# Optimization experiments

Hardware: AMD Instinct MI355X
Metric: run time of the kernel (lower is better)

Reference implementation:

```python
import jax, jax.numpy as jnp
import numpy as np

TAU_PRE = 2.0   # pre-synaptic trace time constant
SCALE = 1.0     # forward(scale=1.0) default
SPIKE_P = 0.1   # firing probability for realistic binary spike trains


def setup_inputs() -> dict:
    key = jax.random.key(0)
    k1, k2 = jax.random.split(key)
    T, B, NIN, NOUT = 2048, 128, 256, 128
    # binary spike trains, [T, B, N]
    in_spikes = (jax.random.uniform(k1, (T, B, NIN)) < SPIKE_P).astype(jnp.float32)
    out_spikes = (jax.random.uniform(k2, (T, B, NOUT)) < SPIKE_P).astype(jnp.float32)
    return {"in_spikes": in_spikes, "out_spikes": out_spikes}


def reference(in_spikes, out_spikes):
    # STDP.forward: loop over recorded timesteps, per step:
    #   trace_pre = trace_pre - trace_pre/tau_pre + in_spike          (decayed trace)
    #   dw = sum_b trace_pre[b, :] (outer) out_spike[b, :] -> [NOUT, NIN]
    #   delta_w += scale * dw
    # Expressed as a single lax.scan over the time axis.
    B, NIN = in_spikes.shape[1], in_spikes.shape[2]
    NOUT = out_spikes.shape[2]

    def step(carry, xs):
        trace_pre, delta_w = carry
        s_in, s_out = xs                                 # [B, NIN], [B, NOUT]
        trace_pre = trace_pre - trace_pre / TAU_PRE + s_in
        dw = jnp.einsum('bi,bo->oi', trace_pre, s_out)   # [NOUT, NIN]
        return (trace_pre, delta_w + SCALE * dw), None

    init = (jnp.zeros((B, NIN), in_spikes.dtype),
            jnp.zeros((NOUT, NIN), in_spikes.dtype))
    (_, delta_w), _ = jax.lax.scan(step, init, (in_spikes, out_spikes))
    return delta_w
```

## Files before the change

### kernel.cpp

```cpp
#include <hip/hip_runtime.h>
#include <hip/hip_bf16.h>

#define T_TOTAL 2048
#define BATCH   128
#define NIN     256
#define NOUT    128

#define TC      256
#define BC      4
#define WARM    32
#define NTC     (T_TOTAL / TC)
#define NBC     (BATCH / BC)
#define NBLOCKS (NTC * NBC)
#define SUP     16
#define NSUP    (TC / SUP)

#define OUT_ELEMS (NOUT * NIN)

typedef __attribute__((ext_vector_type(8)))  __bf16 bf16x8;
typedef __attribute__((ext_vector_type(2)))  __bf16 bf16x2;
typedef __attribute__((ext_vector_type(16))) float  f32x16;
typedef __attribute__((ext_vector_type(4)))  unsigned uint32x4;

static __device__ __forceinline__ unsigned pack_bf16(float a, float b) {
    bf16x2 v = { (__bf16)a, (__bf16)b };
    union { bf16x2 v; unsigned u; } c; c.v = v; return c.u;
}

__global__ __launch_bounds__(512, 2)
void stdp_main(const float* __restrict__ in, const float* __restrict__ outs,
               float* __restrict__ dst, int nslots, int use_atomic)
{
    __shared__ __align__(16) unsigned tr_lds[2][NIN * 32];
    __shared__ __align__(16) unsigned ot_lds[2][NOUT * 32];

    const int tid = threadIdx.x;
    const int bc  = blockIdx.x % NBC;
    const int tc  = blockIdx.x / NBC;
    const int b0  = bc * BC;
    const int t0  = tc * TC;

    const int i_idx = tid & 255;
    const int bh    = tid >> 8;
    const int o_idx = tid & 127;
    const int bp    = (tid >> 7) & 1;
    const int th    = (tid >> 8) & 1;

    float tr0 = 0.f, tr1 = 0.f;

    if (tc > 0) {
        for (int t = t0 - WARM; t < t0; t += 8) {
            float v0[8], v1[8];
#pragma unroll
            for (int u = 0; u < 8; ++u) {
                const size_t base = ((size_t)(t + u) * BATCH + b0 + 2 * bh) * NIN + i_idx;
                v0[u] = in[base];
                v1[u] = in[base + NIN];
            }
#pragma unroll
            for (int u = 0; u < 8; ++u) {
                tr0 = 0.5f * tr0 + v0[u];
                tr1 = 0.5f * tr1 + v1[u];
            }
        }
    }

    f32x16 acc[4];
#pragma unroll
    for (int j = 0; j < 4; ++j) acc[j] = (f32x16)(0.f);

    const int lane  = tid & 63;
    const int wv    = tid >> 6;
    const int mt    = wv & 3;
    const int ntb   = (wv >> 2) * 4;
    const int l31   = lane & 31;
    const int khalf = lane >> 5;
    const int sw    = l31 & 7;

    for (int sg = 0; sg < NSUP; ++sg) {
        const int ts  = t0 + sg * SUP;
        const int buf = sg & 1;

        float vin0[SUP], vin1[SUP];
#pragma unroll
        for (int s = 0; s < SUP; ++s) {
            const size_t base = ((size_t)(ts + s) * BATCH + b0 + 2 * bh) * NIN + i_idx;
            vin0[s] = in[base];
            vin1[s] = in[base + NIN];
        }
        float vo0[8], vo1[8];
#pragma unroll
        for (int u = 0; u < 8; ++u) {
            const size_t baseO = ((size_t)(ts + th * 8 + u) * BATCH + b0 + 2 * bp) * NOUT + o_idx;
            vo0[u] = outs[baseO];
            vo1[u] = outs[baseO + NOUT];
        }

#pragma unroll
        for (int s16 = 0; s16 < 4; ++s16) {
            unsigned bw[4];
#pragma unroll
            for (int q = 0; q < 4; ++q) {
                const int s = s16 * 4 + q;
                tr0 = 0.5f * tr0 + vin0[s];
                tr1 = 0.5f * tr1 + vin1[s];
                bw[q] = pack_bf16(tr0, tr1);
            }
            const int p = (s16 * 2 + bh) ^ (i_idx & 7);
            *(uint32x4*)&tr_lds[buf][i_idx * 32 + p * 4] = (uint32x4){bw[0], bw[1], bw[2], bw[3]};
        }

#pragma unroll
        for (int e = 0; e < 2; ++e) {
            const int s16 = th * 2 + e;
            unsigned aw[4];
#pragma unroll
            for (int q = 0; q < 4; ++q) {
                const int u = e * 4 + q;
                aw[q] = pack_bf16(vo0[u], vo1[u]);
            }
            const int p = (s16 * 2 + bp) ^ (o_idx & 7);
            *(uint32x4*)&ot_lds[buf][o_idx * 32 + p * 4] = (uint32x4){aw[0], aw[1], aw[2], aw[3]};
        }

        __syncthreads();

#pragma unroll
        for (int s16 = 0; s16 < 4; ++s16) {
            const int pc = (s16 * 2 + khalf) ^ sw;
            const bf16x8 a = *(const bf16x8*)&ot_lds[buf][(mt * 32 + l31) * 32 + pc * 4];
#pragma unroll
            for (int j = 0; j < 4; ++j) {
                const int row = (ntb + j) * 32 + l31;
                const bf16x8 b = *(const bf16x8*)&tr_lds[buf][row * 32 + pc * 4];
                acc[j] = __builtin_amdgcn_mfma_f32_32x32x16_bf16(a, b, acc[j], 0, 0, 0);
            }
        }
    }

    float* base = dst + (size_t)(use_atomic ? (blockIdx.x % nslots) : blockIdx.x) * OUT_ELEMS;
#pragma unroll
    for (int j = 0; j < 4; ++j) {
        const int icol = (ntb + j) * 32 + l31;
#pragma unroll
        for (int r = 0; r < 16; ++r) {
            const int row = (r & 3) + 8 * (r >> 2) + 4 * khalf;
            const int o   = mt * 32 + row;
            const float v = acc[j][r];
            if (use_atomic) atomicAdd(&base[o * NIN + icol], v);
            else            base[o * NIN + icol] = v;
        }
    }
}

__global__ void zero_kernel(float* p, int n) {
    int i = blockIdx.x * blockDim.x + threadIdx.x;
    if (i < n) p[i] = 0.f;
}

__global__ __launch_bounds__(256)
void reduce_kernel(const float* __restrict__ ws, float* __restrict__ outp, int nslots) {
    const int idx = blockIdx.x * 256 + threadIdx.x;
    float s = 0.f;
    int k = 0;
    for (; k + 16 <= nslots; k += 16) {
        float v[16];
#pragma unroll
        for (int u = 0; u < 16; ++u) v[u] = ws[(size_t)(k + u) * OUT_ELEMS + idx];
#pragma unroll
        for (int u = 0; u < 16; ++u) s += v[u];
    }
    for (; k < nslots; ++k) s += ws[(size_t)k * OUT_ELEMS + idx];
    outp[idx] = s;
}

extern "C" void kernel_launch(void* const* d_in, const int* in_sizes, int n_in,
                              void* d_out, int out_size, void* d_ws, size_t ws_size,
                              hipStream_t stream) {
    const float* in   = (const float*)d_in[0];
    const float* outs = (const float*)d_in[1];
    float* out = (float*)d_out;
    float* ws  = (float*)d_ws;

    const size_t slot_bytes = (size_t)OUT_ELEMS * sizeof(float);

    if (ws_size >= (size_t)NBLOCKS * slot_bytes) {
        stdp_main<<<NBLOCKS, 512, 0, stream>>>(in, outs, ws, NBLOCKS, 0);
        reduce_kernel<<<OUT_ELEMS / 256, 256, 0, stream>>>(ws, out, NBLOCKS);
    } else if (ws_size >= 16 * slot_bytes) {
        zero_kernel<<<(16 * OUT_ELEMS + 255) / 256, 256, 0, stream>>>(ws, 16 * OUT_ELEMS);
        stdp_main<<<NBLOCKS, 512, 0, stream>>>(in, outs, ws, 16, 1);
        reduce_kernel<<<OUT_ELEMS / 256, 256, 0, stream>>>(ws, out, 16);
    } else {
        zero_kernel<<<(OUT_ELEMS + 255) / 256, 256, 0, stream>>>(out, OUT_ELEMS);
        stdp_main<<<NBLOCKS, 512, 0, stream>>>(in, outs, out, 1, 1);
    }
}
```

Before: 456.6 us.

## Split NIN across two blocks and specialize waves for trace vs out-spike staging

```diff
diff --git a/kernel.cpp b/kernel.cpp
--- a/kernel.cpp
+++ b/kernel.cpp
@@ -11,11 +11,13 @@
 #define WARM    32
 #define NTC     (T_TOTAL / TC)
 #define NBC     (BATCH / BC)
-#define NBLOCKS (NTC * NBC)
+#define NTB     (NTC * NBC)
+#define NBLOCKS (NTB * 2)
 #define SUP     16
 #define NSUP    (TC / SUP)
 
-#define OUT_ELEMS (NOUT * NIN)
+#define OUT_ELEMS  (NOUT * NIN)
+#define SLOT_ELEMS (NOUT * 128)
 
 typedef __attribute__((ext_vector_type(8)))  __bf16 bf16x8;
 typedef __attribute__((ext_vector_type(2)))  __bf16 bf16x2;
@@ -27,33 +29,41 @@
     union { bf16x2 v; unsigned u; } c; c.v = v; return c.u;
 }
 
-__global__ __launch_bounds__(512, 2)
+__global__ __launch_bounds__(512, 4)
 void stdp_main(const float* __restrict__ in, const float* __restrict__ outs,
                float* __restrict__ dst, int nslots, int use_atomic)
 {
-    __shared__ __align__(16) unsigned tr_lds[2][NIN * 32];
-    __shared__ __align__(16) unsigned ot_lds[2][NOUT * 32];
+    __shared__ __align__(16) unsigned tr_lds[2][128 * 32];
+    __shared__ __align__(16) unsigned ot_lds[2][128 * 32];
 
     const int tid = threadIdx.x;
-    const int bc  = blockIdx.x % NBC;
-    const int tc  = blockIdx.x / NBC;
+    const int tb  = blockIdx.x & 255;
+    const int ih  = blockIdx.x >> 8;
+    const int bc  = tb & 31;
+    const int tc  = tb >> 5;
     const int b0  = bc * BC;
     const int t0  = tc * TC;
-
-    const int i_idx = tid & 255;
-    const int bh    = tid >> 8;
-    const int o_idx = tid & 127;
-    const int bp    = (tid >> 7) & 1;
-    const int th    = (tid >> 8) & 1;
+    const int ibase = ih * 128;
+
+    const int wv   = tid >> 6;
+    const bool isB = (wv < 4);
+    const int r7   = tid & 127;
+    const int bp   = (tid >> 7) & 1;
+
+    const int lane  = tid & 63;
+    const int l31   = lane & 31;
+    const int khalf = lane >> 5;
+    const int mt    = wv & 3;
+    const int ntb2  = (wv >> 2) * 2;
 
     float tr0 = 0.f, tr1 = 0.f;
 
-    if (tc > 0) {
+    if (isB && tc > 0) {
         for (int t = t0 - WARM; t < t0; t += 8) {
             float v0[8], v1[8];
 #pragma unroll
             for (int u = 0; u < 8; ++u) {
-                const size_t base = ((size_t)(t + u) * BATCH + b0 + 2 * bh) * NIN + i_idx;
+                const size_t base = ((size_t)(t + u) * BATCH + b0 + 2 * bp) * NIN + ibase + r7;
                 v0[u] = in[base];
                 v1[u] = in[base + NIN];
             }
@@ -65,90 +75,91 @@
         }
     }
 
-    f32x16 acc[4];
-#pragma unroll
-    for (int j = 0; j < 4; ++j) acc[j] = (f32x16)(0.f);
-
-    const int lane  = tid & 63;
-    const int wv    = tid >> 6;
-    const int mt    = wv & 3;
-    const int ntb   = (wv >> 2) * 4;
-    const int l31   = lane & 31;
-    const int khalf = lane >> 5;
-    const int sw    = l31 & 7;
+    f32x16 acc[2];
+    acc[0] = (f32x16)(0.f);
+    acc[1] = (f32x16)(0.f);
 
     for (int sg = 0; sg < NSUP; ++sg) {
         const int ts  = t0 + sg * SUP;
         const int buf = sg & 1;
 
-        float vin0[SUP], vin1[SUP];
-#pragma unroll
-        for (int s = 0; s < SUP; ++s) {
-            const size_t base = ((size_t)(ts + s) * BATCH + b0 + 2 * bh) * NIN + i_idx;
-            vin0[s] = in[base];
-            vin1[s] = in[base + NIN];
-        }
-        float vo0[8], vo1[8];
-#pragma unroll
-        for (int u = 0; u < 8; ++u) {
-            const size_t baseO = ((size_t)(ts + th * 8 + u) * BATCH + b0 + 2 * bp) * NOUT + o_idx;
-            vo0[u] = outs[baseO];
-            vo1[u] = outs[baseO + NOUT];
-        }
+        if (isB) {
+            float v0[SUP], v1[SUP];
+#pragma unroll
+            for (int s = 0; s < SUP; ++s) {
+                const size_t base = ((size_t)(ts + s) * BATCH + b0 + 2 * bp) * NIN + ibase + r7;
+                v0[s] = in[base];
+                v1[s] = in[base + NIN];
+            }
+#pragma unroll
+            for (int s16 = 0; s16 < 4; ++s16) {
+                unsigned w[4];
+#pragma unroll
+                for (int q = 0; q < 4; ++q) {
+                    const int s = s16 * 4 + q;
+                    tr0 = 0.5f * tr0 + v0[s];
+                    tr1 = 0.5f * tr1 + v1[s];
+                    w[q] = pack_bf16(tr0, tr1);
+                }
+                const int p = (s16 * 2 + bp) ^ (r7 & 7);
+                *(uint32x4*)&tr_lds[buf][r7 * 32 + p * 4] = (uint32x4){w[0], w[1], w[2], w[3]};
+            }
+        } else {
+            float v0[SUP], v1[SUP];
+#pragma unroll
+            for (int s = 0; s < SUP; ++s) {
+                const size_t base = ((size_t)(ts + s) * BATCH + b0 + 2 * bp) * NOUT + r7;
+                v0[s] = outs[base];
+                v1[s] = outs[base + NOUT];
+            }
+#pragma unroll
+            for (int s16 = 0; s16 < 4; ++s16) {
+                unsigned w[4];
+#pragma unroll
+                for (int q = 0; q < 4; ++q) {
+                    const int s = s16 * 4 + q;
+                    w[q] = pack_bf16(v0[s], v1[s]);
+                }
+                const int p = (s16 * 2 + bp) ^ (r7 & 7);
+                *(uint32x4*)&ot_lds[buf][r7 * 32 + p * 4] = (uint32x4){w[0], w[1], w[2], w[3]};
+            }
+        }
+
+        __syncthreads();
 
 #pragma unroll
         for (int s16 = 0; s16 < 4; ++s16) {
-            unsigned bw[4];
-#pragma unroll
-            for (int q = 0; q < 4; ++q) {
-                const int s = s16 * 4 + q;
-                tr0 = 0.5f * tr0 + vin0[s];
-                tr1 = 0.5f * tr1 + vin1[s];
-                bw[q] = pack_bf16(tr0, tr1);
-            }
-            const int p = (s16 * 2 + bh) ^ (i_idx & 7);
-            *(uint32x4*)&tr_lds[buf][i_idx * 32 + p * 4] = (uint32x4){bw[0], bw[1], bw[2], bw[3]};
-        }
-
-#pragma unroll
-        for (int e = 0; e < 2; ++e) {
-            const int s16 = th * 2 + e;
-            unsigned aw[4];
-#pragma unroll
-            for (int q = 0; q < 4; ++q) {
-                const int u = e * 4 + q;
-                aw[q] = pack_bf16(vo0[u], vo1[u]);
-            }
-            const int p = (s16 * 2 + bp) ^ (o_idx & 7);
-            *(uint32x4*)&ot_lds[buf][o_idx * 32 + p * 4] = (uint32x4){aw[0], aw[1], aw[2], aw[3]};
-        }
-
-        __syncthreads();
-
-#pragma unroll
-        for (int s16 = 0; s16 < 4; ++s16) {
-            const int pc = (s16 * 2 + khalf) ^ sw;
+            const int pc = (s16 * 2 + khalf) ^ (l31 & 7);
             const bf16x8 a = *(const bf16x8*)&ot_lds[buf][(mt * 32 + l31) * 32 + pc * 4];
 #pragma unroll
-            for (int j = 0; j < 4; ++j) {
-                const int row = (ntb + j) * 32 + l31;
-                const bf16x8 b = *(const bf16x8*)&tr_lds[buf][row * 32 + pc * 4];
+            for (int j = 0; j < 2; ++j) {
+                const bf16x8 b = *(const bf16x8*)&tr_lds[buf][((ntb2 + j) * 32 + l31) * 32 + pc * 4];
                 acc[j] = __builtin_amdgcn_mfma_f32_32x32x16_bf16(a, b, acc[j], 0, 0, 0);
             }
         }
     }
 
-    float* base = dst + (size_t)(use_atomic ? (blockIdx.x % nslots) : blockIdx.x) * OUT_ELEMS;
-#pragma unroll
-    for (int j = 0; j < 4; ++j) {
-        const int icol = (ntb + j) * 32 + l31;
-#pragma unroll
-        for (int r = 0; r < 16; ++r) {
-            const int row = (r & 3) + 8 * (r >> 2) + 4 * khalf;
-            const int o   = mt * 32 + row;
-            const float v = acc[j][r];
-            if (use_atomic) atomicAdd(&base[o * NIN + icol], v);
-            else            base[o * NIN + icol] = v;
+    if (use_atomic) {
+        float* base = dst + (size_t)(blockIdx.x % nslots) * OUT_ELEMS;
+#pragma unroll
+        for (int j = 0; j < 2; ++j) {
+            const int icol = ibase + (ntb2 + j) * 32 + l31;
+#pragma unroll
+            for (int r = 0; r < 16; ++r) {
+                const int row = (r & 3) + 8 * (r >> 2) + 4 * khalf;
+                atomicAdd(&base[(mt * 32 + row) * NIN + icol], acc[j][r]);
+            }
+        }
+    } else {
+        float* base = dst + (size_t)blockIdx.x * SLOT_ELEMS;
+#pragma unroll
+        for (int j = 0; j < 2; ++j) {
+            const int icol = (ntb2 + j) * 32 + l31;
+#pragma unroll
+            for (int r = 0; r < 16; ++r) {
+                const int row = (r & 3) + 8 * (r >> 2) + 4 * khalf;
+                base[(mt * 32 + row) * 128 + icol] = acc[j][r];
+            }
         }
     }
 }
@@ -159,18 +170,29 @@
 }
 
 __global__ __launch_bounds__(256)
-void reduce_kernel(const float* __restrict__ ws, float* __restrict__ outp, int nslots) {
+void reduce_kernel(const float* __restrict__ ws, float* __restrict__ outp) {
+    const int idx = blockIdx.x * 256 + threadIdx.x;
+    const int i  = idx & 255;
+    const int o  = idx >> 8;
+    const int ih = i >> 7;
+    const int i7 = i & 127;
+    const size_t off = (size_t)(ih * 256) * SLOT_ELEMS + o * 128 + i7;
+    float s = 0.f;
+    for (int k = 0; k < 256; k += 16) {
+        float v[16];
+#pragma unroll
+        for (int u = 0; u < 16; ++u) v[u] = ws[off + (size_t)(k + u) * SLOT_ELEMS];
+#pragma unroll
+        for (int u = 0; u < 16; ++u) s += v[u];
+    }
+    outp[idx] = s;
+}
+
+__global__ __launch_bounds__(256)
+void reduce_slots_kernel(const float* __restrict__ ws, float* __restrict__ outp, int nslots) {
     const int idx = blockIdx.x * 256 + threadIdx.x;
     float s = 0.f;
-    int k = 0;
-    for (; k + 16 <= nslots; k += 16) {
-        float v[16];
-#pragma unroll
-        for (int u = 0; u < 16; ++u) v[u] = ws[(size_t)(k + u) * OUT_ELEMS + idx];
-#pragma unroll
-        for (int u = 0; u < 16; ++u) s += v[u];
-    }
-    for (; k < nslots; ++k) s += ws[(size_t)k * OUT_ELEMS + idx];
+    for (int k = 0; k < nslots; ++k) s += ws[(size_t)k * OUT_ELEMS + idx];
     outp[idx] = s;
 }
 
@@ -182,15 +204,13 @@
     float* out = (float*)d_out;
     float* ws  = (float*)d_ws;
 
-    const size_t slot_bytes = (size_t)OUT_ELEMS * sizeof(float);
-
-    if (ws_size >= (size_t)NBLOCKS * slot_bytes) {
+    if (ws_size >= (size_t)NBLOCKS * SLOT_ELEMS * sizeof(float)) {
         stdp_main<<<NBLOCKS, 512, 0, stream>>>(in, outs, ws, NBLOCKS, 0);
-        reduce_kernel<<<OUT_ELEMS / 256, 256, 0, stream>>>(ws, out, NBLOCKS);
-    } else if (ws_size >= 16 * slot_bytes) {
+        reduce_kernel<<<OUT_ELEMS / 256, 256, 0, stream>>>(ws, out);
+    } else if (ws_size >= 16 * (size_t)OUT_ELEMS * sizeof(float)) {
         zero_kernel<<<(16 * OUT_ELEMS + 255) / 256, 256, 0, stream>>>(ws, 16 * OUT_ELEMS);
         stdp_main<<<NBLOCKS, 512, 0, stream>>>(in, outs, ws, 16, 1);
-        reduce_kernel<<<OUT_ELEMS / 256, 256, 0, stream>>>(ws, out, 16);
+        reduce_slots_kernel<<<OUT_ELEMS / 256, 256, 0, stream>>>(ws, out, 16);
     } else {
         zero_kernel<<<(OUT_ELEMS + 255) / 256, 256, 0, stream>>>(out, OUT_ELEMS);
         stdp_main<<<NBLOCKS, 512, 0, stream>>>(in, outs, out, 1, 1);
```

Measured after the change: 508.4 us. +11.3%, slower.
